# Optimization experiments

Measured on AMD Instinct MI355X. Metric: run time of the kernel, lower is better.

Reference implementation:

```python
import jax, jax.numpy as jnp
import numpy as np

B, S, D = 1, 2048, 512
H, KH, DH = 8, 2, 64
G = H // KH            # grouped queries per kv head
CBS = SBS = 32         # compress / selection block size (equal)
NSEL = 8               # num selected blocks
WIN = 128              # sliding window size
NC = S // CBS          # num compressed blocks
NF = S // SBS          # num fine blocks (S divisible by SBS)
CDIM = CBS * DH


def setup_inputs():
    key = jax.random.key(0)
    ks = jax.random.split(key, 12)
    r = lambda k, shape, s=0.02: jax.random.normal(k, shape, dtype=jnp.float32) * s
    return {
        "inp": jax.random.normal(ks[0], (B, S, D), dtype=jnp.float32),
        "norm_w": jnp.ones((D,), jnp.float32),
        "w_qkv": r(ks[1], (D, H * DH + 2 * KH * DH)),
        "mem_kv": r(ks[2], (2, KH, 1, DH)),
        "k_pos": r(ks[3], (KH, CBS, DH)),
        "v_pos": r(ks[4], (KH, CBS, DH)),
        "kc_w1": r(ks[5], (CDIM, CDIM)), "kc_b1": jnp.zeros((CDIM,), jnp.float32),
        "kc_w2": r(ks[6], (CDIM, DH)), "kc_b2": jnp.zeros((DH,), jnp.float32),
        "vc_w1": r(ks[7], (CDIM, CDIM)), "vc_b1": jnp.zeros((CDIM,), jnp.float32),
        "vc_w2": r(ks[8], (CDIM, DH)), "vc_b2": jnp.zeros((DH,), jnp.float32),
        "comb_w": r(ks[9], (D, 3 * H)),
        "comb_b": jnp.tile(jnp.array([-2.0, -2.0, 2.0], jnp.float32), H),
        "out_w": r(ks[10], (H * DH, D)),
    }


def _rope(x):  # x: [b, h, n, d]; interleaved rotary (rotary-embedding-torch style)
    d, n = x.shape[-1], x.shape[-2]
    inv = 1.0 / (10000.0 ** (jnp.arange(0, d, 2, dtype=jnp.float32) / d))
    fr = jnp.arange(n, dtype=jnp.float32)[:, None] * inv[None, :]  # [n, d/2]
    fr = jnp.repeat(fr, 2, axis=-1)                                 # [n, d]
    cos, sin = jnp.cos(fr), jnp.sin(fr)
    xp = x.reshape(*x.shape[:-1], d // 2, 2)
    xr = jnp.stack((-xp[..., 1], xp[..., 0]), axis=-1).reshape(x.shape)
    return x * cos + xr * sin


def _mlp(x, w1, b1, w2, b2):
    return jax.nn.relu(x @ w1 + b1) @ w2 + b2


def _forward(inp, norm_w, w_qkv, mem_kv, k_pos, v_pos, kc_w1, kc_b1, kc_w2, kc_b2,
             vc_w1, vc_b1, vc_w2, vc_b2, comb_w, comb_b, out_w):
    scale = DH ** -0.5
    NEG = -jnp.finfo(jnp.float32).max

    # RMSNorm
    x = inp * jax.lax.rsqrt(jnp.mean(inp * inp, -1, keepdims=True)
                            + jnp.finfo(jnp.float32).eps) * norm_w

    qkv = x @ w_qkv
    q, k, v = jnp.split(qkv, [H * DH, H * DH + KH * DH], axis=-1)
    q = q.reshape(B, S, H, DH).transpose(0, 2, 1, 3)    # b h n d
    k = k.reshape(B, S, KH, DH).transpose(0, 2, 1, 3)   # b kh n d
    v = v.reshape(B, S, KH, DH).transpose(0, 2, 1, 3)

    # --- 1. compressed attention (unrotated q/k) ---
    kb = k.reshape(B, KH, NC, CBS, DH) + k_pos[None, :, None]
    vb = v.reshape(B, KH, NC, CBS, DH) + v_pos[None, :, None]
    ck = _mlp(kb.reshape(B, KH, NC, CDIM), kc_w1, kc_b1, kc_w2, kc_b2)  # b kh nc d
    cv = _mlp(vb.reshape(B, KH, NC, CDIM), vc_w1, vc_b1, vc_w2, vc_b2)
    ck = jnp.concatenate((jnp.broadcast_to(mem_kv[0][None], (B, KH, 1, DH)), ck), axis=2)
    cv = jnp.concatenate((jnp.broadcast_to(mem_kv[1][None], (B, KH, 1, DH)), cv), axis=2)

    ck_pos = jnp.concatenate((jnp.array([-1]), (jnp.arange(NC) + 1) * CBS - 1))
    cmask = ck_pos[None, :] < jnp.arange(S)[:, None]     # [S, 1+NC]

    qg = q.reshape(B, KH, G, S, DH)
    csim = jnp.einsum('bhgid,bhjd->bhgij', qg, ck) * scale
    csim = jnp.where(cmask, csim, NEG)
    cattn = jax.nn.softmax(csim, axis=-1)
    c_out = jnp.einsum('bhgij,bhjd->bhgid', cattn, cv)   # b kh g n d

    # --- importance scores -> top-k block selection (shared across grouped queries) ---
    imp = csim[..., 1:].mean(axis=2)                     # b kh n nc
    imp = jnp.pad(imp, ((0, 0), (0, 0), (0, 0), (1, 0)), constant_values=-1e3)
    imp = jax.nn.softmax(imp, axis=-1)[..., 1:]
    sel_val, sel_idx = jax.lax.top_k(imp, NSEL)          # b kh n sel

    # --- rotary for fine + sliding branches ---
    qr, kr = _rope(q), _rope(k)

    # --- 2. fine (selected-block) attention ---
    own = jnp.broadcast_to((jnp.arange(S) // SBS)[None, None, :, None], (B, KH, S, 1))
    sel_idx = jnp.concatenate((sel_idx, own), axis=-1)   # b kh n (sel+1), own block appended

    bmask = jnp.broadcast_to((sel_val > 1e-10)[..., None], (B, KH, S, NSEL, SBS))
    tri = jnp.tril(jnp.ones((SBS, SBS), bool))
    diag = jnp.broadcast_to(jnp.tile(tri, (NF, 1))[None, None, :, None, :], (B, KH, S, 1, SBS))
    fmask = jnp.concatenate((bmask, diag), axis=-2).reshape(B, KH, 1, S, (NSEL + 1) * SBS)

    kfb = kr.reshape(B, KH, NF, SBS, DH)
    vfb = v.reshape(B, KH, NF, SBS, DH)
    gidx = sel_idx[..., None, None]                      # b kh n sel1 1 1
    fk = jnp.take_along_axis(kfb[:, :, None], gidx, axis=3).reshape(B, KH, S, (NSEL + 1) * SBS, DH)
    fv = jnp.take_along_axis(vfb[:, :, None], gidx, axis=3).reshape(B, KH, S, (NSEL + 1) * SBS, DH)

    fqg = qr.reshape(B, KH, G, S, DH)
    fsim = jnp.einsum('bhgid,bhijd->bhgij', fqg, fk) * scale
    fsim = jnp.where(fmask, fsim, NEG)
    fattn = jax.nn.softmax(fsim, axis=-1)
    f_out = jnp.einsum('bhgij,bhijd->bhgid', fattn, fv)  # b kh g n d

    diff = jnp.arange(S)[:, None] - jnp.arange(S)[None, :]
    smask = (diff >= 0) & (diff <= WIN)
    ssim = jnp.einsum('bhgid,bhjd->bhgij', fqg, kr) * scale
    ssim = jnp.where(smask, ssim, NEG)
    sattn = jax.nn.softmax(ssim, axis=-1)
    s_out = jnp.einsum('bhgij,bhjd->bhgid', sattn, v)    # b kh g n d

    # --- learned gating combine over [compressed, fine, sliding] ---
    gates = jax.nn.sigmoid(x @ comb_w + comb_b).reshape(B, S, H, 3)
    gates = gates.transpose(0, 2, 1, 3).reshape(B, KH, G, S, 3)
    out = gates[..., 0:1] * c_out + gates[..., 1:2] * f_out + gates[..., 2:3] * s_out
    out = out.reshape(B, H, S, DH).transpose(0, 2, 1, 3).reshape(B, S, H * DH)
    return out @ out_w


def reference(inp, norm_w, w_qkv, mem_kv, k_pos, v_pos, kc_w1, kc_b1, kc_w2, kc_b2,
              vc_w1, vc_b1, vc_w2, vc_b2, comb_w, comb_b, out_w):
    return _forward(inp, norm_w, w_qkv, mem_kv, k_pos, v_pos, kc_w1, kc_b1, kc_w2, kc_b2,
                    vc_w1, vc_b1, vc_w2, vc_b2, comb_w, comb_b, out_w)
```

## Files before the change

kernel.cpp:

```cpp
#include <hip/hip_runtime.h>
#include <hip/hip_bf16.h>
#include <math.h>

#define S 2048
#define D 512
#define H 8
#define KH 2
#define DH 64
#define G 4
#define CBS 32
#define NSEL 8
#define WIN 128
#define NC 64
#define CDIM 2048

typedef __attribute__((ext_vector_type(8))) short bf16x8_t;
typedef __attribute__((ext_vector_type(4))) float f32x4_t;
typedef __attribute__((ext_vector_type(2))) _Float16 half2v;

static __device__ __forceinline__ unsigned short f2bf(float f) {
    union { float f; unsigned int u; } v; v.f = f;
    unsigned int r = (v.u + 0x7FFFu + ((v.u >> 16) & 1u)) >> 16;
    return (unsigned short)r;
}
static __device__ __forceinline__ float bf2f(unsigned short h) {
    union { unsigned int u; float f; } v; v.u = ((unsigned int)h) << 16;
    return v.f;
}
static __device__ __forceinline__ float bflo(unsigned int u) {
    union { unsigned int u; float f; } v; v.u = u << 16; return v.f;
}
static __device__ __forceinline__ float bfhi(unsigned int u) {
    union { unsigned int u; float f; } v; v.u = u & 0xffff0000u; return v.f;
}
static __device__ __forceinline__ unsigned short f2h(float f) {
    union { _Float16 h; unsigned short s; } v; v.h = (_Float16)f; return v.s;
}
static __device__ __forceinline__ float h2f(unsigned short u) {
    union { unsigned short s; _Float16 h; } v; v.s = u; return (float)v.h;
}
static __device__ __forceinline__ float dot2f16(unsigned int a, unsigned int b, float c) {
    union { unsigned int u; half2v h; } A, B; A.u = a; B.u = b;
    return __builtin_amdgcn_fdot2(A.h, B.h, c, false);
}

__global__ __launch_bounds__(256) void k_prep(const float* __restrict__ inp,
                                              const float* __restrict__ w,
                                              unsigned short* __restrict__ xbf,
                                              float* __restrict__ ct, float* __restrict__ st) {
    int b = blockIdx.x, t = threadIdx.x;
    if (b < S) {
        const float* row = inp + (size_t)b * D;
        float a = row[t], c = row[t + 256];
        float ss = a * a + c * c;
        for (int off = 32; off; off >>= 1) ss += __shfl_xor(ss, off);
        __shared__ float red[4];
        if ((t & 63) == 0) red[t >> 6] = ss;
        __syncthreads();
        float tot = red[0] + red[1] + red[2] + red[3];
        float inv = rsqrtf(tot / (float)D + 1.1920929e-07f);
        xbf[(size_t)b * D + t]       = f2bf(a * inv * w[t]);
        xbf[(size_t)b * D + t + 256] = f2bf(c * inv * w[t + 256]);
    } else {
        int idx = (b - S) * 256 + t;
        int s = idx >> 5, p = idx & 31;
        float inv = powf(10000.0f, -(float)p / 32.0f);
        float fr = (float)s * inv;
        ct[idx] = cosf(fr); st[idx] = sinf(fr);
    }
}

__global__ __launch_bounds__(256) void k_gemm0(
    const unsigned short* __restrict__ A,
    const float* __restrict__ W,
    const float* __restrict__ k_pos, const float* __restrict__ v_pos,
    const float* __restrict__ ct, const float* __restrict__ st,
    unsigned short* __restrict__ q16,
    unsigned short* __restrict__ qr16, unsigned short* __restrict__ kr16,
    unsigned short* __restrict__ v16, unsigned short* __restrict__ kbvb)
{
    const int K = 512, N = 768;
    __shared__ __align__(16) unsigned short As[64][40];
    __shared__ __align__(16) unsigned short Bs[64][40];
    int t = threadIdx.x;
    int m0 = blockIdx.y * 64, n0 = blockIdx.x * 64;
    int wave = t >> 6, lane = t & 63;
    int mh = wave & 1, nh = wave >> 1;
    f32x4_t acc[2][2] = {};
    int ar = t >> 2, ac = (t & 3) * 8;
    int bk = t >> 3, bn = (t & 7) * 8;
    int arow_l = lane & 15, kcol = (lane >> 4) * 8;
    uint4 aReg = *(const uint4*)&A[(size_t)(m0 + ar) * K + ac];
    const float4* wr = (const float4*)&W[(size_t)bk * N + n0 + bn];
    float4 w0 = wr[0], w1 = wr[1];
    for (int k0 = 0; k0 < K; k0 += 32) {
        __syncthreads();
        *(uint4*)&As[ar][ac] = aReg;
        unsigned short bp[8];
        bp[0] = f2bf(w0.x); bp[1] = f2bf(w0.y); bp[2] = f2bf(w0.z); bp[3] = f2bf(w0.w);
        bp[4] = f2bf(w1.x); bp[5] = f2bf(w1.y); bp[6] = f2bf(w1.z); bp[7] = f2bf(w1.w);
        #pragma unroll
        for (int j = 0; j < 8; ++j) Bs[bn + j][bk] = bp[j];
        __syncthreads();
        if (k0 + 32 < K) {
            aReg = *(const uint4*)&A[(size_t)(m0 + ar) * K + k0 + 32 + ac];
            wr = (const float4*)&W[(size_t)(k0 + 32 + bk) * N + n0 + bn];
            w0 = wr[0]; w1 = wr[1];
        }
        bf16x8_t a0 = *(const bf16x8_t*)&As[mh * 32 + arow_l][kcol];
        bf16x8_t a1 = *(const bf16x8_t*)&As[mh * 32 + 16 + arow_l][kcol];
        bf16x8_t b0v = *(const bf16x8_t*)&Bs[nh * 32 + arow_l][kcol];
        bf16x8_t b1v = *(const bf16x8_t*)&Bs[nh * 32 + 16 + arow_l][kcol];
        acc[0][0] = __builtin_amdgcn_mfma_f32_16x16x32_bf16(a0, b0v, acc[0][0], 0, 0, 0);
        acc[0][1] = __builtin_amdgcn_mfma_f32_16x16x32_bf16(a0, b1v, acc[0][1], 0, 0, 0);
        acc[1][0] = __builtin_amdgcn_mfma_f32_16x16x32_bf16(a1, b0v, acc[1][0], 0, 0, 0);
        acc[1][1] = __builtin_amdgcn_mfma_f32_16x16x32_bf16(a1, b1v, acc[1][1], 0, 0, 0);
    }
    #pragma unroll
    for (int mi = 0; mi < 2; ++mi)
    #pragma unroll
    for (int ni = 0; ni < 2; ++ni)
    #pragma unroll
    for (int r = 0; r < 4; ++r) {
        int gm = m0 + mh * 32 + mi * 16 + (lane >> 4) * 4 + r;
        int gn = n0 + nh * 32 + ni * 16 + (lane & 15);
        float val = acc[mi][ni][r];
        float part = __shfl_xor(val, 1);
        if (gn < 512) {
            int hh = gn >> 6, d = gn & 63;
            size_t idx = ((size_t)hh * S + gm) * DH + d;
            q16[idx] = f2h(val);
            int p = d >> 1;
            float cc = ct[gm * 32 + p], sn = st[gm * 32 + p];
            float y = (d & 1) ? (val * cc + part * sn) : (val * cc - part * sn);
            qr16[idx] = f2h(y);
        } else if (gn < 640) {
            int gk = gn - 512, khh = gk >> 6, d = gk & 63;
            size_t idx = ((size_t)khh * S + gm) * DH + d;
            int p = d >> 1;
            float cc = ct[gm * 32 + p], sn = st[gm * 32 + p];
            float y = (d & 1) ? (val * cc + part * sn) : (val * cc - part * sn);
            kr16[idx] = f2h(y);
            int tt = gm & 31, nc2 = gm >> 5;
            kbvb[((size_t)(khh * 64 + nc2)) * 2048 + tt * 64 + d] =
                f2bf(val + k_pos[(khh * CBS + tt) * 64 + d]);
        } else {
            int gv = gn - 640, khh = gv >> 6, d = gv & 63;
            size_t idx = ((size_t)khh * S + gm) * DH + d;
            v16[idx] = f2bf(val);
            int tt = gm & 31, nc2 = gm >> 5;
            kbvb[((size_t)(128 + khh * 64 + nc2)) * 2048 + tt * 64 + d] =
                f2bf(val + v_pos[(khh * CBS + tt) * 64 + d]);
        }
    }
}

template<int MODE>
__global__ __launch_bounds__(256) void k_gemm(
    const unsigned short* __restrict__ A,
    const float* __restrict__ B0,
    int M, int N, int K,
    float* __restrict__ outC)
{
    __shared__ __align__(16) unsigned short As[64][40];
    __shared__ __align__(16) unsigned short Bs[64][40];
    int t = threadIdx.x;
    int m0 = blockIdx.y * 64, n0 = blockIdx.x * 64;
    const float* W = B0;
    int wave = t >> 6, lane = t & 63;
    int mh = wave & 1, nh = wave >> 1;
    f32x4_t acc[2][2] = {};
    int ar = t >> 2, ac = (t & 3) * 8;
    int bk = t >> 3, bn = (t & 7) * 8;
    int arow_l = lane & 15, kcol = (lane >> 4) * 8;
    uint4 aReg = *(const uint4*)&A[(size_t)(m0 + ar) * K + ac];
    const float4* wr = (const float4*)&W[(size_t)bk * N + n0 + bn];
    float4 w0 = wr[0], w1 = wr[1];
    for (int k0 = 0; k0 < K; k0 += 32) {
        __syncthreads();
        *(uint4*)&As[ar][ac] = aReg;
        unsigned short bp[8];
        bp[0] = f2bf(w0.x); bp[1] = f2bf(w0.y); bp[2] = f2bf(w0.z); bp[3] = f2bf(w0.w);
        bp[4] = f2bf(w1.x); bp[5] = f2bf(w1.y); bp[6] = f2bf(w1.z); bp[7] = f2bf(w1.w);
        #pragma unroll
        for (int j = 0; j < 8; ++j) Bs[bn + j][bk] = bp[j];
        __syncthreads();
        if (k0 + 32 < K) {
            aReg = *(const uint4*)&A[(size_t)(m0 + ar) * K + k0 + 32 + ac];
            wr = (const float4*)&W[(size_t)(k0 + 32 + bk) * N + n0 + bn];
            w0 = wr[0]; w1 = wr[1];
        }
        bf16x8_t a0 = *(const bf16x8_t*)&As[mh * 32 + arow_l][kcol];
        bf16x8_t a1 = *(const bf16x8_t*)&As[mh * 32 + 16 + arow_l][kcol];
        bf16x8_t b0v = *(const bf16x8_t*)&Bs[nh * 32 + arow_l][kcol];
        bf16x8_t b1v = *(const bf16x8_t*)&Bs[nh * 32 + 16 + arow_l][kcol];
        acc[0][0] = __builtin_amdgcn_mfma_f32_16x16x32_bf16(a0, b0v, acc[0][0], 0, 0, 0);
        acc[0][1] = __builtin_amdgcn_mfma_f32_16x16x32_bf16(a0, b1v, acc[0][1], 0, 0, 0);
        acc[1][0] = __builtin_amdgcn_mfma_f32_16x16x32_bf16(a1, b0v, acc[1][0], 0, 0, 0);
        acc[1][1] = __builtin_amdgcn_mfma_f32_16x16x32_bf16(a1, b1v, acc[1][1], 0, 0, 0);
    }
    #pragma unroll
    for (int mi = 0; mi < 2; ++mi)
    #pragma unroll
    for (int ni = 0; ni < 2; ++ni)
    #pragma unroll
    for (int r = 0; r < 4; ++r) {
        int gm = m0 + mh * 32 + mi * 16 + (lane >> 4) * 4 + r;
        int gn = n0 + nh * 32 + ni * 16 + (lane & 15);
        outC[(size_t)gm * N + gn] = acc[mi][ni][r];
    }
}

__global__ __launch_bounds__(256) void k_gemm1p(
    const unsigned short* __restrict__ A,
    const float* __restrict__ kc_w1, const float* __restrict__ vc_w1,
    float* __restrict__ part)
{
    const int N = 2048, LDA = 2048;
    __shared__ __align__(16) unsigned short As[64][40];
    __shared__ __align__(16) unsigned short Bs[64][40];
    int t = threadIdx.x;
    int mb = blockIdx.y & 3, ks = blockIdx.y >> 2;
    int m0 = mb * 64, n0 = blockIdx.x * 64, kbeg = ks * 1024;
    const float* W = (mb >= 2) ? vc_w1 : kc_w1;
    int wave = t >> 6, lane = t & 63;
    int mh = wave & 1, nh = wave >> 1;
    f32x4_t acc[2][2] = {};
    int ar = t >> 2, ac = (t & 3) * 8;
    int bk = t >> 3, bn = (t & 7) * 8;
    int arow_l = lane & 15, kcol = (lane >> 4) * 8;
    uint4 aReg = *(const uint4*)&A[(size_t)(m0 + ar) * LDA + kbeg + ac];
    const float4* wr = (const float4*)&W[(size_t)(kbeg + bk) * N + n0 + bn];
    float4 w0 = wr[0], w1 = wr[1];
    for (int k0 = 0; k0 < 1024; k0 += 32) {
        __syncthreads();
        *(uint4*)&As[ar][ac] = aReg;
        unsigned short bp[8];
        bp[0] = f2bf(w0.x); bp[1] = f2bf(w0.y); bp[2] = f2bf(w0.z); bp[3] = f2bf(w0.w);
        bp[4] = f2bf(w1.x); bp[5] = f2bf(w1.y); bp[6] = f2bf(w1.z); bp[7] = f2bf(w1.w);
        #pragma unroll
        for (int j = 0; j < 8; ++j) Bs[bn + j][bk] = bp[j];
        __syncthreads();
        if (k0 + 32 < 1024) {
            aReg = *(const uint4*)&A[(size_t)(m0 + ar) * LDA + kbeg + k0 + 32 + ac];
            wr = (const float4*)&W[(size_t)(kbeg + k0 + 32 + bk) * N + n0 + bn];
            w0 = wr[0]; w1 = wr[1];
        }
        bf16x8_t a0 = *(const bf16x8_t*)&As[mh * 32 + arow_l][kcol];
        bf16x8_t a1 = *(const bf16x8_t*)&As[mh * 32 + 16 + arow_l][kcol];
        bf16x8_t b0v = *(const bf16x8_t*)&Bs[nh * 32 + arow_l][kcol];
        bf16x8_t b1v = *(const bf16x8_t*)&Bs[nh * 32 + 16 + arow_l][kcol];
        acc[0][0] = __builtin_amdgcn_mfma_f32_16x16x32_bf16(a0, b0v, acc[0][0], 0, 0, 0);
        acc[0][1] = __builtin_amdgcn_mfma_f32_16x16x32_bf16(a0, b1v, acc[0][1], 0, 0, 0);
        acc[1][0] = __builtin_amdgcn_mfma_f32_16x16x32_bf16(a1, b0v, acc[1][0], 0, 0, 0);
        acc[1][1] = __builtin_amdgcn_mfma_f32_16x16x32_bf16(a1, b1v, acc[1][1], 0, 0, 0);
    }
    #pragma unroll
    for (int mi = 0; mi < 2; ++mi)
    #pragma unroll
    for (int ni = 0; ni < 2; ++ni)
    #pragma unroll
    for (int r = 0; r < 4; ++r) {
        int gm = m0 + mh * 32 + mi * 16 + (lane >> 4) * 4 + r;
        int gn = n0 + nh * 32 + ni * 16 + (lane & 15);
        part[((size_t)ks * 256 + gm) * N + gn] = acc[mi][ni][r];
    }
}

__global__ __launch_bounds__(256) void k_mlp2p(
    const float* __restrict__ g1part,
    const float* __restrict__ kc_b1, const float* __restrict__ vc_b1,
    const float* __restrict__ kc_w2, const float* __restrict__ vc_w2,
    float* __restrict__ part)
{
    const int N = 64, LDA = 2048;
    __shared__ __align__(16) unsigned short As[64][40];
    __shared__ __align__(16) unsigned short Bs[64][40];
    int t = threadIdx.x;
    int ks = blockIdx.x, m0 = blockIdx.y * 64;
    int kbeg = ks * 512;
    const float* W  = (blockIdx.y >= 2) ? vc_w2 : kc_w2;
    const float* b1 = (m0 >= 128) ? vc_b1 : kc_b1;
    int wave = t >> 6, lane = t & 63;
    int mh = wave & 1, nh = wave >> 1;
    f32x4_t acc[2][2] = {};
    int ar = t >> 2, ac = (t & 3) * 8;
    int bk = t >> 3, bn = (t & 7) * 8;
    int arow_l = lane & 15, kcol = (lane >> 4) * 8;
    int arow = m0 + ar;
    const float4* p0 = (const float4*)&g1part[(size_t)arow * LDA + kbeg + ac];
    const float4* p1 = (const float4*)&g1part[(size_t)(256 + arow) * LDA + kbeg + ac];
    const float4* bb = (const float4*)&b1[kbeg + ac];
    float4 x0 = p0[0], x1 = p0[1], y0 = p1[0], y1 = p1[1], c0 = bb[0], c1 = bb[1];
    const float4* wr = (const float4*)&W[(size_t)(kbeg + bk) * N + bn];
    float4 w0 = wr[0], w1 = wr[1];
    for (int k0 = 0; k0 < 512; k0 += 32) {
        __syncthreads();
        {
            unsigned short ap[8];
            ap[0] = f2bf(fmaxf(x0.x + y0.x + c0.x, 0.f));
            ap[1] = f2bf(fmaxf(x0.y + y0.y + c0.y, 0.f));
            ap[2] = f2bf(fmaxf(x0.z + y0.z + c0.z, 0.f));
            ap[3] = f2bf(fmaxf(x0.w + y0.w + c0.w, 0.f));
            ap[4] = f2bf(fmaxf(x1.x + y1.x + c1.x, 0.f));
            ap[5] = f2bf(fmaxf(x1.y + y1.y + c1.y, 0.f));
            ap[6] = f2bf(fmaxf(x1.z + y1.z + c1.z, 0.f));
            ap[7] = f2bf(fmaxf(x1.w + y1.w + c1.w, 0.f));
            *(uint4*)&As[ar][ac] = *(const uint4*)ap;
        }
        unsigned short bp[8];
        bp[0] = f2bf(w0.x); bp[1] = f2bf(w0.y); bp[2] = f2bf(w0.z); bp[3] = f2bf(w0.w);
        bp[4] = f2bf(w1.x); bp[5] = f2bf(w1.y); bp[6] = f2bf(w1.z); bp[7] = f2bf(w1.w);
        #pragma unroll
        for (int j = 0; j < 8; ++j) Bs[bn + j][bk] = bp[j];
        __syncthreads();
        if (k0 + 32 < 512) {
            int kk2 = kbeg + k0 + 32 + ac;
            p0 = (const float4*)&g1part[(size_t)arow * LDA + kk2];
            p1 = (const float4*)&g1part[(size_t)(256 + arow) * LDA + kk2];
            bb = (const float4*)&b1[kk2];
            x0 = p0[0]; x1 = p0[1]; y0 = p1[0]; y1 = p1[1]; c0 = bb[0]; c1 = bb[1];
            wr = (const float4*)&W[(size_t)(kbeg + k0 + 32 + bk) * N + bn];
            w0 = wr[0]; w1 = wr[1];
        }
        bf16x8_t a0 = *(const bf16x8_t*)&As[mh * 32 + arow_l][kcol];
        bf16x8_t a1 = *(const bf16x8_t*)&As[mh * 32 + 16 + arow_l][kcol];
        bf16x8_t b0v = *(const bf16x8_t*)&Bs[nh * 32 + arow_l][kcol];
        bf16x8_t b1v = *(const bf16x8_t*)&Bs[nh * 32 + 16 + arow_l][kcol];
        acc[0][0] = __builtin_amdgcn_mfma_f32_16x16x32_bf16(a0, b0v, acc[0][0], 0, 0, 0);
        acc[0][1] = __builtin_amdgcn_mfma_f32_16x16x32_bf16(a0, b1v, acc[0][1], 0, 0, 0);
        acc[1][0] = __builtin_amdgcn_mfma_f32_16x16x32_bf16(a1, b0v, acc[1][0], 0, 0, 0);
        acc[1][1] = __builtin_amdgcn_mfma_f32_16x16x32_bf16(a1, b1v, acc[1][1], 0, 0, 0);
    }
    #pragma unroll
    for (int mi = 0; mi < 2; ++mi)
    #pragma unroll
    for (int ni = 0; ni < 2; ++ni)
    #pragma unroll
    for (int r = 0; r < 4; ++r) {
        int gm = m0 + mh * 32 + mi * 16 + (lane >> 4) * 4 + r;
        int gn = nh * 32 + ni * 16 + (lane & 15);
        part[((size_t)ks * 256 + gm) * 64 + gn] = acc[mi][ni][r];
    }
}

__global__ __launch_bounds__(256) void k_mlp2r(
    const float* __restrict__ part, const float* __restrict__ kc_b2,
    const float* __restrict__ vc_b2, const float* __restrict__ mem_kv,
    unsigned short* __restrict__ ck16, float* __restrict__ cv)
{
    int idx = blockIdx.x * 256 + threadIdx.x;
    int gm = idx >> 6, gn = idx & 63;
    float sum = part[(size_t)gm * 64 + gn] + part[(size_t)(256 + gm) * 64 + gn]
              + part[(size_t)(512 + gm) * 64 + gn] + part[(size_t)(768 + gm) * 64 + gn];
    bool isv = gm >= 128;
    sum += isv ? vc_b2[gn] : kc_b2[gn];
    int kh2 = (gm >> 6) & 1, nc2 = gm & 63;
    if (isv) cv[(kh2 * 65 + 1 + nc2) * 64 + gn] = sum;
    else     ck16[(kh2 * 65 + 1 + nc2) * 64 + gn] = f2h(sum);
    if (blockIdx.x == 0 && threadIdx.x < 256) {
        int t = threadIdx.x;
        int path2 = t >> 7, khm = (t >> 6) & 1, dm = t & 63;
        float mv = mem_kv[path2 * (KH * DH) + khm * DH + dm];
        if (path2) cv[khm * 65 * 64 + dm] = mv;
        else       ck16[khm * 65 * 64 + dm] = f2h(mv);
    }
}

__global__ __launch_bounds__(256) void k_cattn(
    const unsigned short* __restrict__ q16, const unsigned short* __restrict__ ck16,
    const float* __restrict__ cv,
    float* __restrict__ c_out, int* __restrict__ sel)
{
    int kh = blockIdx.x >> 9, sc = blockIdx.x & 511;
    int s_base = sc * 4;
    __shared__ __align__(16) unsigned char KL[64 * 128];
    __shared__ float cvL[64][66];
    __shared__ unsigned short qL16[4][64];
    __shared__ float simL[4][64];
    __shared__ float pL[4][64];
    int t = threadIdx.x;
    int g = t >> 6, lane = t & 63;
    unsigned short qv0 = q16[((kh * G + g) * S + s_base + 0) * DH + lane];
    unsigned short qv1 = q16[((kh * G + g) * S + s_base + 1) * DH + lane];
    unsigned short qv2 = q16[((kh * G + g) * S + s_base + 2) * DH + lane];
    unsigned short qv3 = q16[((kh * G + g) * S + s_base + 3) * DH + lane];
    {
        int j = t >> 2, gp = (t & 3) * 2;
        const uint4* src = (const uint4*)&ck16[((size_t)kh * 65 + j) * 64];
        uint4 a = src[gp], b = src[gp + 1];
        *(uint4*)(KL + j * 128 + 16 * (gp ^ (j & 7)))       = a;
        *(uint4*)(KL + j * 128 + 16 * ((gp + 1) ^ (j & 7))) = b;
    }
    for (int idx = t; idx < 4096; idx += 256) {
        int j = idx >> 6, d = idx & 63;
        cvL[j][d] = cv[(kh * 65 + j) * 64 + d];
    }
    __syncthreads();
    for (int si = 0; si < 4; ++si) {
        int s = s_base + si;
        qL16[g][lane] = (si == 0) ? qv0 : (si == 1) ? qv1 : (si == 2) ? qv2 : qv3;
        int j = lane;
        bool valid = (j == 0) || (s >= j * 32);
        float sva = 0.f, svb = 0.f, svc = 0.f, svd = 0.f;
        #pragma unroll
        for (int grp = 0; grp < 8; ++grp) {
            uint4 kk = *(const uint4*)(KL + j * 128 + 16 * (grp ^ (j & 7)));
            uint4 qq = *(const uint4*)((const unsigned char*)qL16 + g * 128 + 16 * grp);
            sva = dot2f16(kk.x, qq.x, sva);
            svb = dot2f16(kk.y, qq.y, svb);
            svc = dot2f16(kk.z, qq.z, svc);
            svd = dot2f16(kk.w, qq.w, svd);
        }
        float sim = ((sva + svb) + (svc + svd)) * 0.125f;
        float simm = valid ? sim : -INFINITY;
        simL[g][j] = simm;
        float m = simm;
        for (int off = 32; off; off >>= 1) m = fmaxf(m, __shfl_xor(m, off));
        float p = valid ? __expf(simm - m) : 0.f;
        float den = p;
        for (int off = 32; off; off >>= 1) den += __shfl_xor(den, off);
        pL[g][j] = p / den;
        float acc = 0.f;
        #pragma unroll
        for (int j4 = 0; j4 < 16; ++j4) {
            float4 p4 = *(const float4*)&pL[g][j4 * 4];
            acc += p4.x * cvL[j4 * 4 + 0][lane] + p4.y * cvL[j4 * 4 + 1][lane]
                 + p4.z * cvL[j4 * 4 + 2][lane] + p4.w * cvL[j4 * 4 + 3][lane];
        }
        c_out[((kh * G + g) * S + s) * DH + lane] = acc;
        __syncthreads();
        if (g == 0) {
            int l = lane;
            float lv = -INFINITY;
            if (l < 63 && s >= (l + 1) * 32)
                lv = 0.25f * (simL[0][l + 1] + simL[1][l + 1] + simL[2][l + 1] + simL[3][l + 1]);
            float mm = lv;
            for (int off = 32; off; off >>= 1) mm = fmaxf(mm, __shfl_xor(mm, off));
            mm = fmaxf(mm, -1000.0f);
            float e = (lv == -INFINITY) ? 0.f : __expf(lv - mm);
            float dd = e;
            for (int off = 32; off; off >>= 1) dd += __shfl_xor(dd, off);
            dd += __expf(-1000.0f - mm);
            float val = e / dd;
            pL[0][l] = val;
            int rk = 0;
            #pragma unroll
            for (int j4 = 0; j4 < 16; ++j4) {
                float4 v4 = *(const float4*)&pL[0][j4 * 4];
                const float* vv = (const float*)&v4;
                #pragma unroll
                for (int q2 = 0; q2 < 4; ++q2) {
                    int i2 = j4 * 4 + q2;
                    rk += (vv[q2] > val || (vv[q2] == val && i2 < l)) ? 1 : 0;
                }
            }
            int base = (kh * S + s) * 9;
            if (rk < 8) sel[base + rk] = (val > 1e-10f) ? l : -1;
            if (l == 0) sel[base + 8] = s >> 5;
        }
        __syncthreads();
    }
}

__global__ __launch_bounds__(256, 4) void k_swattn(
    const unsigned short* __restrict__ qr16, const unsigned short* __restrict__ kr16,
    const unsigned short* __restrict__ v16, const int* __restrict__ sel,
    float* __restrict__ fob, float* __restrict__ sob)
{
    int kh = blockIdx.x >> 11, s = blockIdx.x & 2047;
    int t = threadIdx.x, w = t >> 6, lane = t & 63, g = w;
    __shared__ __align__(16) unsigned char KL[2][64 * 128];
    __shared__ __align__(16) unsigned char VL[2][64 * 144];
    __shared__ float pL[4][64];

    const uint4* qp = (const uint4*)&qr16[(((size_t)kh * G + g) * S + s) * DH];
    uint4 qq0 = qp[0], qq1 = qp[1], qq2 = qp[2], qq3 = qp[3];
    uint4 qq4 = qp[4], qq5 = qp[5], qq6 = qp[6], qq7 = qp[7];

    int base = (kh * S + s) * 9;
    int lo = s - WIN; if (lo < 0) lo = 0;

    int nv = 0;
    #pragma unroll
    for (int i = 0; i < 8; ++i) nv += (sel[base + i] >= 0) ? 1 : 0;
    int npairF = (nv + 1) >> 1;
    int nchS = (s - lo + 63) >> 6;
    int nch = npairF + nchS;
    int ownStart = s & ~31;
    bool hasOwn = (s & 31) != 0;

    float lF = 0.f, lS = 0.f;
    float a0F = 0.f, a1F = 0.f, a0S = 0.f, a1S = 0.f;
    int h = lane >> 5, dhalf = lane & 31;
    int key = w * 16 + (lane & 15);
    int grpA = lane >> 4;
    uint4 z = make_uint4(0, 0, 0, 0);
    uint4 kd0 = z, kd1 = z, vd0 = z, vd1 = z;

    auto issue = [&](int c) {
        int gkey; bool kv;
        if (c < npairF) {
            int b = sel[base + 2 * c + ((key >> 5) & 1)];
            kv = b >= 0;
            gkey = (kv ? b : 0) * 32 + (key & 31);
        } else {
            gkey = lo + (c - npairF) * 64 + key;
            kv = gkey < s;
        }
        const uint4* kp = (const uint4*)&kr16[((size_t)kh * S + gkey) * DH];
        const uint4* vp = (const uint4*)&v16 [((size_t)kh * S + gkey) * DH];
        kd0 = kv ? kp[grpA] : z;
        kd1 = kv ? kp[grpA + 4] : z;
        vd0 = kv ? vp[grpA] : z;
        vd1 = kv ? vp[grpA + 4] : z;
    };
    auto stage = [&](int buf) {
        *(uint4*)(KL[buf] + key * 128 + 16 * (grpA ^ (key & 7))) = kd0;
        *(uint4*)(KL[buf] + key * 128 + 16 * ((grpA + 4) ^ (key & 7))) = kd1;
        *(uint4*)(VL[buf] + key * 144 + 16 * grpA) = vd0;
        *(uint4*)(VL[buf] + key * 144 + 16 * (grpA + 4)) = vd1;
    };

    issue(0);
    stage(0);
    if (nch > 1) issue(1);
    __syncthreads();

    for (int c = 0; c < nch; ++c) {
        const unsigned char* KLc = KL[c & 1];
        const unsigned char* VLc = VL[c & 1];

        int j = lane;
        bool isPair = c < npairF;
        int cs = c - npairF;
        int gk0 = lo + cs * 64;
        bool valid = isPair ? ((j < 32) || ((2 * c + 1) < nv))
                            : ((gk0 + j) < s);

        float sva = 0.f, svb = 0.f, svc = 0.f, svd = 0.f;
        #define QKSTEP(G_, QQ_) { \
            uint4 kk = *(const uint4*)(KLc + j * 128 + 16 * ((G_) ^ (j & 7))); \
            sva = dot2f16(kk.x, QQ_.x, sva); svb = dot2f16(kk.y, QQ_.y, svb); \
            svc = dot2f16(kk.z, QQ_.z, svc); svd = dot2f16(kk.w, QQ_.w, svd); }
        QKSTEP(0, qq0) QKSTEP(1, qq1) QKSTEP(2, qq2) QKSTEP(3, qq3)
        QKSTEP(4, qq4) QKSTEP(5, qq5) QKSTEP(6, qq6) QKSTEP(7, qq7)
        #undef QKSTEP
        float sv = (sva + svb) + (svc + svd);
        float p = valid ? __expf(sv * 0.125f) : 0.f;
        pL[g][j] = p;

        bool doOwn = (!isPair) && hasOwn && (cs == nchS - 1);
        if (!doOwn) {
            if (isPair) lF += p; else lS += p;
            float t0 = 0.f, t1 = 0.f;
            #pragma unroll
            for (int j4 = 0; j4 < 8; ++j4) {
                float4 p4 = *(const float4*)&pL[g][h * 32 + j4 * 4];
                const float* pp = (const float*)&p4;
                #pragma unroll
                for (int q2 = 0; q2 < 4; ++q2) {
                    unsigned int v2 = *(const unsigned int*)(VLc + (h * 32 + j4 * 4 + q2) * 144 + 4 * dhalf);
                    t0 += pp[q2] * bflo(v2);
                    t1 += pp[q2] * bfhi(v2);
                }
            }
            if (isPair) { a0F += t0; a1F += t1; }
            else        { a0S += t0; a1S += t1; }
        } else {
            lS += p;
            int jstart = ownStart - gk0;
            if (j >= jstart) lF += p;
            float pre0 = 0.f, pre1 = 0.f, suf0 = 0.f, suf1 = 0.f;
            #pragma unroll
            for (int j4 = 0; j4 < 8; ++j4) {
                float4 p4 = *(const float4*)&pL[g][h * 32 + j4 * 4];
                const float* pp = (const float*)&p4;
                #pragma unroll
                for (int q2 = 0; q2 < 4; ++q2) {
                    int jj = h * 32 + j4 * 4 + q2;
                    unsigned int v2 = *(const unsigned int*)(VLc + jj * 144 + 4 * dhalf);
                    float t0 = pp[q2] * bflo(v2);
                    float t1 = pp[q2] * bfhi(v2);
                    bool inSuf = jj >= jstart;
                    suf0 += inSuf ? t0 : 0.f;
                    suf1 += inSuf ? t1 : 0.f;
                    pre0 += inSuf ? 0.f : t0;
                    pre1 += inSuf ? 0.f : t1;
                }
            }
            a0S += pre0 + suf0; a1S += pre1 + suf1;
            a0F += suf0;        a1F += suf1;
        }

        if (c + 1 < nch) {
            stage((c + 1) & 1);
            if (c + 2 < nch) issue(c + 2);
        }
        __syncthreads();
    }
    {
        float qd = h2f(qr16[(((size_t)kh * G + g) * S + s) * DH + lane]);
        float pr = qd * h2f(kr16[((size_t)kh * S + s) * DH + lane]);
        for (int off = 32; off; off >>= 1) pr += __shfl_xor(pr, off);
        float pd = __expf(pr * 0.125f);
        for (int off = 32; off; off >>= 1) {
            lF += __shfl_xor(lF, off);
            lS += __shfl_xor(lS, off);
        }
        lF += pd; lS += pd;
        if (h == 0) {
            unsigned int v2 = *(const unsigned int*)&v16[(((size_t)kh * S + s) * DH) + 2 * dhalf];
            float b0 = bflo(v2), b1 = bfhi(v2);
            a0F += pd * b0; a1F += pd * b1;
            a0S += pd * b0; a1S += pd * b1;
        }
    }
    a0F += __shfl_xor(a0F, 32);
    a1F += __shfl_xor(a1F, 32);
    a0S += __shfl_xor(a0S, 32);
    a1S += __shfl_xor(a1S, 32);
    if (lane < 32) {
        size_t ob = (((size_t)kh * G + g) * S + s) * DH + 2 * dhalf;
        float invF = 1.f / lF, invS = 1.f / lS;
        *(float2*)&fob[ob] = make_float2(a0F * invF, a1F * invF);
        *(float2*)&sob[ob] = make_float2(a0S * invS, a1S * invS);
    }
}

__global__ __launch_bounds__(256) void k_combine(
    const unsigned short* __restrict__ xbf, const float* __restrict__ comb_w, const float* __restrict__ comb_b,
    const float* __restrict__ c_out, const float* __restrict__ f_out, const float* __restrict__ s_out,
    unsigned short* __restrict__ comb)
{
    int s = blockIdx.x, t = threadIdx.x;
    __shared__ float gpart[24][8];
    __shared__ float gates[24];
    if (t < 192) {
        int cc = t >> 3, pt = t & 7;
        float sum = 0.f;
        for (int d = pt * 64; d < pt * 64 + 64; ++d)
            sum += bf2f(xbf[s * D + d]) * comb_w[d * 24 + cc];
        gpart[cc][pt] = sum;
    }
    __syncthreads();
    if (t < 24) {
        float sum = comb_b[t];
        for (int i = 0; i < 8; ++i) sum += gpart[t][i];
        gates[t] = 1.f / (1.f + __expf(-sum));
    }
    __syncthreads();
    for (int o = t; o < 512; o += 256) {
        int h = o >> 6, d = o & 63;
        int idx = (h * S + s) * DH + d;
        float r = gates[h * 3] * c_out[idx] + gates[h * 3 + 1] * f_out[idx] + gates[h * 3 + 2] * s_out[idx];
        comb[s * D + o] = f2bf(r);
    }
}

extern "C" void kernel_launch(void* const* d_in, const int* in_sizes, int n_in,
                              void* d_out, int out_size, void* d_ws, size_t ws_size,
                              hipStream_t stream)
{
    (void)in_sizes; (void)n_in; (void)out_size; (void)ws_size;
    const float* inp    = (const float*)d_in[0];
    const float* norm_w = (const float*)d_in[1];
    const float* w_qkv  = (const float*)d_in[2];
    const float* mem_kv = (const float*)d_in[3];
    const float* k_pos  = (const float*)d_in[4];
    const float* v_pos  = (const float*)d_in[5];
    const float* kc_w1  = (const float*)d_in[6];
    const float* kc_b1  = (const float*)d_in[7];
    const float* kc_w2  = (const float*)d_in[8];
    const float* kc_b2  = (const float*)d_in[9];
    const float* vc_w1  = (const float*)d_in[10];
    const float* vc_b1  = (const float*)d_in[11];
    const float* vc_w2  = (const float*)d_in[12];
    const float* vc_b2  = (const float*)d_in[13];
    const float* comb_w = (const float*)d_in[14];
    const float* comb_b = (const float*)d_in[15];
    const float* out_w  = (const float*)d_in[16];
    float* out = (float*)d_out;

    char* w = (char*)d_ws;
    size_t off = 0;
    auto alloc = [&](size_t bytes) { void* p = w + off; off += (bytes + 255) & ~(size_t)255; return p; };
    unsigned short* xbf   = (unsigned short*)alloc((size_t)S * D * 2);
    unsigned short* kbvb  = (unsigned short*)alloc((size_t)256 * 2048 * 2);
    unsigned short* combb = (unsigned short*)alloc((size_t)S * 512 * 2);
    unsigned short* q16   = (unsigned short*)alloc((size_t)H * S * DH * 2);
    unsigned short* qr16  = (unsigned short*)alloc((size_t)H * S * DH * 2);
    unsigned short* kr16  = (unsigned short*)alloc((size_t)KH * S * DH * 2);
    unsigned short* v16   = (unsigned short*)alloc((size_t)KH * S * DH * 2);
    unsigned short* ck16  = (unsigned short*)alloc((size_t)KH * 65 * 64 * 2);
    float* cvb  = (float*)alloc((size_t)KH * 65 * 64 * 4);
    float* cob  = (float*)alloc((size_t)H * S * DH * 4);
    float* fob  = (float*)alloc((size_t)H * S * DH * 4);
    float* sob  = (float*)alloc((size_t)H * S * DH * 4);
    float* ctab = (float*)alloc((size_t)S * 32 * 4);
    float* stab = (float*)alloc((size_t)S * 32 * 4);
    float* partb = (float*)alloc((size_t)4 * 256 * 64 * 4);
    float* g1part = (float*)alloc((size_t)2 * 256 * 2048 * 4);
    int*   selb = (int*)alloc((size_t)KH * S * 9 * 4);

    k_prep<<<S + 256, 256, 0, stream>>>(inp, norm_w, xbf, ctab, stab);

    k_gemm0<<<dim3(768 / 64, S / 64), 256, 0, stream>>>(
        xbf, w_qkv, k_pos, v_pos, ctab, stab, q16, qr16, kr16, v16, kbvb);

    k_gemm1p<<<dim3(32, 8), 256, 0, stream>>>(kbvb, kc_w1, vc_w1, g1part);

    k_mlp2p<<<dim3(4, 4), 256, 0, stream>>>(g1part, kc_b1, vc_b1, kc_w2, vc_w2, partb);
    k_mlp2r<<<64, 256, 0, stream>>>(partb, kc_b2, vc_b2, mem_kv, ck16, cvb);

    k_cattn<<<KH * 512, 256, 0, stream>>>(q16, ck16, cvb, cob, selb);

    k_swattn<<<KH * S, 256, 0, stream>>>(qr16, kr16, v16, selb, fob, sob);

    k_combine<<<S, 256, 0, stream>>>(xbf, comb_w, comb_b, cob, fob, sob, combb);
    k_gemm<2><<<dim3(512 / 64, S / 64), 256, 0, stream>>>(
        combb, out_w, S, 512, 512, out);
}
```

Before: 202.6 us.

## Store V transposed in fp16 and use packed dot2 for PV accumulation

V is now stored as fp16 instead of bf16 and staged into shared memory transposed (dim-major), with probabilities kept as fp16, so the P·V inner loop can use packed fp16 dot2 instructions over key pairs instead of scalar bf16 unpack and FMA. This cuts ALU work and LDS reads in the sliding/fine attention kernel. In exchange, staging now does scalar 16-bit transposed LDS writes that may cause bank conflicts, and fp16 probabilities and values lose range and precision compared with fp32/bf16.

Result: slower. 331.1 us (+63.4%).

```diff
diff --git a/kernel.cpp b/kernel.cpp
--- a/kernel.cpp
+++ b/kernel.cpp
@@ -147,7 +147,7 @@
         } else {
             int gv = gn - 640, khh = gv >> 6, d = gv & 63;
             size_t idx = ((size_t)khh * S + gm) * DH + d;
-            v16[idx] = f2bf(val);
+            v16[idx] = f2h(val);
             int tt = gm & 31, nc2 = gm >> 5;
             kbvb[((size_t)(128 + khh * 64 + nc2)) * 2048 + tt * 64 + d] =
                 f2bf(val + v_pos[(khh * CBS + tt) * 64 + d]);
@@ -471,8 +471,8 @@
     int kh = blockIdx.x >> 11, s = blockIdx.x & 2047;
     int t = threadIdx.x, w = t >> 6, lane = t & 63, g = w;
     __shared__ __align__(16) unsigned char KL[2][64 * 128];
-    __shared__ __align__(16) unsigned char VL[2][64 * 144];
-    __shared__ float pL[4][64];
+    __shared__ __align__(16) unsigned short VT[2][64][74];
+    __shared__ __align__(16) unsigned short pL2[4][64];
 
     const uint4* qp = (const uint4*)&qr16[(((size_t)kh * G + g) * S + s) * DH];
     uint4 qq0 = qp[0], qq1 = qp[1], qq2 = qp[2], qq3 = qp[3];
@@ -518,8 +518,13 @@
     auto stage = [&](int buf) {
         *(uint4*)(KL[buf] + key * 128 + 16 * (grpA ^ (key & 7))) = kd0;
         *(uint4*)(KL[buf] + key * 128 + 16 * ((grpA + 4) ^ (key & 7))) = kd1;
-        *(uint4*)(VL[buf] + key * 144 + 16 * grpA) = vd0;
-        *(uint4*)(VL[buf] + key * 144 + 16 * (grpA + 4)) = vd1;
+        const unsigned short* pv0 = (const unsigned short*)&vd0;
+        const unsigned short* pv1 = (const unsigned short*)&vd1;
+        #pragma unroll
+        for (int e = 0; e < 8; ++e) {
+            VT[buf][grpA * 8 + e][key]      = pv0[e];
+            VT[buf][grpA * 8 + 32 + e][key] = pv1[e];
+        }
     };
 
     issue(0);
@@ -529,7 +534,7 @@
 
     for (int c = 0; c < nch; ++c) {
         const unsigned char* KLc = KL[c & 1];
-        const unsigned char* VLc = VL[c & 1];
+        const unsigned short (*VTc)[74] = VT[c & 1];
 
         int j = lane;
         bool isPair = c < npairF;
@@ -548,22 +553,20 @@
         #undef QKSTEP
         float sv = (sva + svb) + (svc + svd);
         float p = valid ? __expf(sv * 0.125f) : 0.f;
-        pL[g][j] = p;
+        pL2[g][j] = f2h(p);
 
         bool doOwn = (!isPair) && hasOwn && (cs == nchS - 1);
         if (!doOwn) {
             if (isPair) lF += p; else lS += p;
+            const unsigned int* pw = (const unsigned int*)&pL2[g][h * 32];
+            const unsigned short* vr0 = &VTc[2 * dhalf][h * 32];
+            const unsigned short* vr1 = &VTc[2 * dhalf + 1][h * 32];
             float t0 = 0.f, t1 = 0.f;
             #pragma unroll
-            for (int j4 = 0; j4 < 8; ++j4) {
-                float4 p4 = *(const float4*)&pL[g][h * 32 + j4 * 4];
-                const float* pp = (const float*)&p4;
-                #pragma unroll
-                for (int q2 = 0; q2 < 4; ++q2) {
-                    unsigned int v2 = *(const unsigned int*)(VLc + (h * 32 + j4 * 4 + q2) * 144 + 4 * dhalf);
-                    t0 += pp[q2] * bflo(v2);
-                    t1 += pp[q2] * bfhi(v2);
-                }
+            for (int k2 = 0; k2 < 16; ++k2) {
+                unsigned int pp2 = pw[k2];
+                t0 = dot2f16(pp2, *(const unsigned int*)&vr0[2 * k2], t0);
+                t1 = dot2f16(pp2, *(const unsigned int*)&vr1[2 * k2], t1);
             }
             if (isPair) { a0F += t0; a1F += t1; }
             else        { a0S += t0; a1S += t1; }
@@ -573,21 +576,17 @@
             if (j >= jstart) lF += p;
             float pre0 = 0.f, pre1 = 0.f, suf0 = 0.f, suf1 = 0.f;
             #pragma unroll
-            for (int j4 = 0; j4 < 8; ++j4) {
-                float4 p4 = *(const float4*)&pL[g][h * 32 + j4 * 4];
-                const float* pp = (const float*)&p4;
-                #pragma unroll
-                for (int q2 = 0; q2 < 4; ++q2) {
-                    int jj = h * 32 + j4 * 4 + q2;
-                    unsigned int v2 = *(const unsigned int*)(VLc + jj * 144 + 4 * dhalf);
-                    float t0 = pp[q2] * bflo(v2);
-                    float t1 = pp[q2] * bfhi(v2);
-                    bool inSuf = jj >= jstart;
-                    suf0 += inSuf ? t0 : 0.f;
-                    suf1 += inSuf ? t1 : 0.f;
-                    pre0 += inSuf ? 0.f : t0;
-                    pre1 += inSuf ? 0.f : t1;
-                }
+            for (int jj4 = 0; jj4 < 32; ++jj4) {
+                int jj = h * 32 + jj4;
+                float pj = h2f(pL2[g][jj]);
+                float v0 = h2f(VTc[2 * dhalf][jj]);
+                float v1 = h2f(VTc[2 * dhalf + 1][jj]);
+                float q0 = pj * v0, q1 = pj * v1;
+                bool inSuf = jj >= jstart;
+                suf0 += inSuf ? q0 : 0.f;
+                suf1 += inSuf ? q1 : 0.f;
+                pre0 += inSuf ? 0.f : q0;
+                pre1 += inSuf ? 0.f : q1;
             }
             a0S += pre0 + suf0; a1S += pre1 + suf1;
             a0F += suf0;        a1F += suf1;
@@ -611,7 +610,8 @@
         lF += pd; lS += pd;
         if (h == 0) {
             unsigned int v2 = *(const unsigned int*)&v16[(((size_t)kh * S + s) * DH) + 2 * dhalf];
-            float b0 = bflo(v2), b1 = bfhi(v2);
+            float b0 = h2f((unsigned short)(v2 & 0xffffu));
+            float b1 = h2f((unsigned short)(v2 >> 16));
             a0F += pd * b0; a1F += pd * b1;
             a0S += pd * b0; a1S += pd * b1;
         }
```

## Fuse gated combine into attention kernels and compute gates in separate kernel

Applied to the files above, without the earlier changes.

Gate logits and sigmoid now come from a separate small kernel that runs early. The compressed-attention kernel writes its gated output as bf16 straight into the combined buffer. The sliding/fine-attention kernel then reads that value, adds its own two gated outputs and writes the result back. This removes the three fp32 per-head output buffers and the separate combine kernel's read traffic, in exchange for a bf16 read-modify-write and an extra rounding of the compressed branch before summation.

After: 205.6 us. No clear change (+1.5%).

```diff
diff --git a/kernel.cpp b/kernel.cpp
--- a/kernel.cpp
+++ b/kernel.cpp
@@ -67,6 +67,27 @@
         float inv = powf(10000.0f, -(float)p / 32.0f);
         float fr = (float)s * inv;
         ct[idx] = cosf(fr); st[idx] = sinf(fr);
+    }
+}
+
+__global__ __launch_bounds__(256) void k_gates(
+    const unsigned short* __restrict__ xbf, const float* __restrict__ comb_w,
+    const float* __restrict__ comb_b, float* __restrict__ gates)
+{
+    int s = blockIdx.x, t = threadIdx.x;
+    __shared__ float gpart[24][8];
+    if (t < 192) {
+        int cc = t >> 3, pt = t & 7;
+        float sum = 0.f;
+        for (int d = pt * 64; d < pt * 64 + 64; ++d)
+            sum += bf2f(xbf[s * D + d]) * comb_w[d * 24 + cc];
+        gpart[cc][pt] = sum;
+    }
+    __syncthreads();
+    if (t < 24) {
+        float sum = comb_b[t];
+        for (int i = 0; i < 8; ++i) sum += gpart[t][i];
+        gates[s * 24 + t] = 1.f / (1.f + __expf(-sum));
     }
 }
 
@@ -369,8 +390,8 @@
 
 __global__ __launch_bounds__(256) void k_cattn(
     const unsigned short* __restrict__ q16, const unsigned short* __restrict__ ck16,
-    const float* __restrict__ cv,
-    float* __restrict__ c_out, int* __restrict__ sel)
+    const float* __restrict__ cv, const float* __restrict__ gates,
+    unsigned short* __restrict__ combb, int* __restrict__ sel)
 {
     int kh = blockIdx.x >> 9, sc = blockIdx.x & 511;
     int s_base = sc * 4;
@@ -428,7 +449,9 @@
             acc += p4.x * cvL[j4 * 4 + 0][lane] + p4.y * cvL[j4 * 4 + 1][lane]
                  + p4.z * cvL[j4 * 4 + 2][lane] + p4.w * cvL[j4 * 4 + 3][lane];
         }
-        c_out[((kh * G + g) * S + s) * DH + lane] = acc;
+        int head = kh * G + g;
+        float gC = gates[s * 24 + head * 3];
+        combb[(size_t)s * 512 + head * 64 + lane] = f2bf(gC * acc);
         __syncthreads();
         if (g == 0) {
             int l = lane;
@@ -466,7 +489,7 @@
 __global__ __launch_bounds__(256, 4) void k_swattn(
     const unsigned short* __restrict__ qr16, const unsigned short* __restrict__ kr16,
     const unsigned short* __restrict__ v16, const int* __restrict__ sel,
-    float* __restrict__ fob, float* __restrict__ sob)
+    const float* __restrict__ gates, unsigned short* __restrict__ combb)
 {
     int kh = blockIdx.x >> 11, s = blockIdx.x & 2047;
     int t = threadIdx.x, w = t >> 6, lane = t & 63, g = w;
@@ -621,40 +644,16 @@
     a0S += __shfl_xor(a0S, 32);
     a1S += __shfl_xor(a1S, 32);
     if (lane < 32) {
-        size_t ob = (((size_t)kh * G + g) * S + s) * DH + 2 * dhalf;
+        int head = kh * G + g;
+        size_t cb = (size_t)s * 512 + head * 64 + 2 * dhalf;
+        float gF = gates[s * 24 + head * 3 + 1];
+        float gS = gates[s * 24 + head * 3 + 2];
         float invF = 1.f / lF, invS = 1.f / lS;
-        *(float2*)&fob[ob] = make_float2(a0F * invF, a1F * invF);
-        *(float2*)&sob[ob] = make_float2(a0S * invS, a1S * invS);
-    }
-}
-
-__global__ __launch_bounds__(256) void k_combine(
-    const unsigned short* __restrict__ xbf, const float* __restrict__ comb_w, const float* __restrict__ comb_b,
-    const float* __restrict__ c_out, const float* __restrict__ f_out, const float* __restrict__ s_out,
-    unsigned short* __restrict__ comb)
-{
-    int s = blockIdx.x, t = threadIdx.x;
-    __shared__ float gpart[24][8];
-    __shared__ float gates[24];
-    if (t < 192) {
-        int cc = t >> 3, pt = t & 7;
-        float sum = 0.f;
-        for (int d = pt * 64; d < pt * 64 + 64; ++d)
-            sum += bf2f(xbf[s * D + d]) * comb_w[d * 24 + cc];
-        gpart[cc][pt] = sum;
-    }
-    __syncthreads();
-    if (t < 24) {
-        float sum = comb_b[t];
-        for (int i = 0; i < 8; ++i) sum += gpart[t][i];
-        gates[t] = 1.f / (1.f + __expf(-sum));
-    }
-    __syncthreads();
-    for (int o = t; o < 512; o += 256) {
-        int h = o >> 6, d = o & 63;
-        int idx = (h * S + s) * DH + d;
-        float r = gates[h * 3] * c_out[idx] + gates[h * 3 + 1] * f_out[idx] + gates[h * 3 + 2] * s_out[idx];
-        comb[s * D + o] = f2bf(r);
+        unsigned int cc = *(const unsigned int*)&combb[cb];
+        float r0 = bflo(cc) + gF * (a0F * invF) + gS * (a0S * invS);
+        float r1 = bfhi(cc) + gF * (a1F * invF) + gS * (a1S * invS);
+        unsigned int o = (unsigned)f2bf(r0) | ((unsigned)f2bf(r1) << 16);
+        *(unsigned int*)&combb[cb] = o;
     }
 }
 
@@ -694,17 +693,17 @@
     unsigned short* v16   = (unsigned short*)alloc((size_t)KH * S * DH * 2);
     unsigned short* ck16  = (unsigned short*)alloc((size_t)KH * 65 * 64 * 2);
     float* cvb  = (float*)alloc((size_t)KH * 65 * 64 * 4);
-    float* cob  = (float*)alloc((size_t)H * S * DH * 4);
-    float* fob  = (float*)alloc((size_t)H * S * DH * 4);
-    float* sob  = (float*)alloc((size_t)H * S * DH * 4);
     float* ctab = (float*)alloc((size_t)S * 32 * 4);
     float* stab = (float*)alloc((size_t)S * 32 * 4);
+    float* gatesb = (float*)alloc((size_t)S * 24 * 4);
     float* partb = (float*)alloc((size_t)4 * 256 * 64 * 4);
     float* g1part = (float*)alloc((size_t)2 * 256 * 2048 * 4);
     int*   selb = (int*)alloc((size_t)KH * S * 9 * 4);
 
     k_prep<<<S + 256, 256, 0, stream>>>(inp, norm_w, xbf, ctab, stab);
 
+    k_gates<<<S, 256, 0, stream>>>(xbf, comb_w, comb_b, gatesb);
+
     k_gemm0<<<dim3(768 / 64, S / 64), 256, 0, stream>>>(
         xbf, w_qkv, k_pos, v_pos, ctab, stab, q16, qr16, kr16, v16, kbvb);
 
@@ -713,11 +712,10 @@
     k_mlp2p<<<dim3(4, 4), 256, 0, stream>>>(g1part, kc_b1, vc_b1, kc_w2, vc_w2, partb);
     k_mlp2r<<<64, 256, 0, stream>>>(partb, kc_b2, vc_b2, mem_kv, ck16, cvb);
 
-    k_cattn<<<KH * 512, 256, 0, stream>>>(q16, ck16, cvb, cob, selb);
-
-    k_swattn<<<KH * S, 256, 0, stream>>>(qr16, kr16, v16, selb, fob, sob);
-
-    k_combine<<<S, 256, 0, stream>>>(xbf, comb_w, comb_b, cob, fob, sob, combb);
+    k_cattn<<<KH * 512, 256, 0, stream>>>(q16, ck16, cvb, gatesb, combb, selb);
+
+    k_swattn<<<KH * S, 256, 0, stream>>>(qr16, kr16, v16, selb, gatesb, combb);
+
     k_gemm<2><<<dim3(512 / 64, S / 64), 256, 0, stream>>>(
         combb, out_w, S, 512, 512, out);
 }
```
